# Optimization experiments

Measured on AMD Instinct MI355X. Metric: run time of the kernel, lower is better.

## Reference

```python
import jax, jax.numpy as jnp
import numpy as np

B, N, E = 64, 64, 512          # batch, objects per image, edges per image
OBJ_DIM, Q_DIM, KS = 2048, 1024, 8
HID = Q_DIM // 2               # 512


def setup_inputs() -> dict:
    key = jax.random.key(0)
    k1, k2, k3, k4, k5, k6 = jax.random.split(key, 6)
    node_feats = jax.random.normal(k1, (B, N, OBJ_DIM), jnp.float32)
    q_feats = jax.random.normal(k2, (B, Q_DIM), jnp.float32)
    # Edges: per-image random (i, j) pairs with self-loops removed, indices into
    # the flattened [B*N*N] pairwise tensor, sorted by batch (m//b per image).
    i = jax.random.randint(k3, (B, E), 0, N)
    off = jax.random.randint(k4, (B, E), 1, N)
    j = (i + off) % N
    base = jnp.arange(B)[:, None] * (N * N)
    indexes = (base + i * N + j).reshape(-1).astype(jnp.int32)  # [B*E]
    scale = 0.02
    W_obj = jax.random.normal(k5, (OBJ_DIM, HID), jnp.float32) * scale
    b_obj = jnp.zeros((HID,), jnp.float32)
    W_q = jax.random.normal(k6, (Q_DIM, HID * KS), jnp.float32) * scale
    b_q = jnp.zeros((HID * KS,), jnp.float32)
    return {"node_feats": node_feats, "q_feats": q_feats, "indexes": indexes,
            "W_obj": W_obj, "b_obj": b_obj, "W_q": W_q, "b_q": b_q}


def reference(node_feats, q_feats, indexes, W_obj, b_obj, W_q, b_q):
    b, n, _ = node_feats.shape
    # obj_prob_l: Linear + ReLU -> [B, N, HID]
    node_h = jax.nn.relu(jnp.einsum('bno,oh->bnh', node_feats, W_obj) + b_obj)
    hid = node_h.shape[-1]
    # node_intersect(method='sum') then gather via graph.indexes:
    # equivalent to gathering (i, j) pairs directly instead of materializing [B*N*N, HID]
    bidx = indexes // (n * n)
    rem = indexes % (n * n)
    src = rem // n
    dst = rem % n
    obj_e = node_h[bidx, src] + node_h[bidx, dst]            # [M, HID]
    # q_prob_l: Linear + ReLU -> [B, HID*KS], viewed as per-edge kernels [M, HID, KS]
    q_h = jax.nn.relu(q_feats @ W_q + b_q)                   # [B, HID*KS]
    ks = q_h.shape[-1] // hid
    q_e = q_h.reshape(b, hid, ks)[bidx]                      # [M, HID, KS]
    # batched (1,HID) @ (HID,KS) dot product, then divide by per-kernel norm
    edge_logit = jnp.einsum('mh,mhk->mk', obj_e, q_e)        # [M, KS]
    edge_logit = edge_logit / jnp.linalg.norm(q_e, axis=1)   # [M, KS]
    return edge_logit
```

## Files before the change

kernel.cpp:

```cpp
#include <hip/hip_runtime.h>
#include <hip/hip_bf16.h>


using bf16x8 = __attribute__((ext_vector_type(8))) __bf16;
using f32x4  = __attribute__((ext_vector_type(4))) float;

__device__ __forceinline__ unsigned short f2bf(float f) {
    unsigned int u = __float_as_uint(f);
    unsigned int r = (u + 0x7FFFu + ((u >> 16) & 1u)) >> 16;
    return (unsigned short)r;
}

__device__ __forceinline__ uint4 pk8u(f32x4 a, f32x4 b) {
    union { unsigned short us[8]; uint4 u4; } r;
    r.us[0] = f2bf(a[0]); r.us[1] = f2bf(a[1]); r.us[2] = f2bf(a[2]); r.us[3] = f2bf(a[3]);
    r.us[4] = f2bf(b[0]); r.us[5] = f2bf(b[1]); r.us[6] = f2bf(b[2]); r.us[7] = f2bf(b[3]);
    return r.u4;
}

__device__ __forceinline__ bf16x8 pk8(f32x4 a, f32x4 b) {
    union { uint4 u4; bf16x8 v; } r;
    r.u4 = pk8u(a, b);
    return r.v;
}

__device__ __forceinline__ void gl_lds16(const void* g, void* l) {
    __builtin_amdgcn_global_load_lds(
        (const __attribute__((address_space(1))) unsigned int*)g,
        (__attribute__((address_space(3))) unsigned int*)l,
        16, 0, 0);
}

__global__ __launch_bounds__(256) void cvt_k(const float* __restrict__ nf,
                                             const float* __restrict__ W,
                                             unsigned short* __restrict__ A,
                                             unsigned short* __restrict__ WT) {
    __shared__ float lds[32][33];
    int bid = blockIdx.x;
    if (bid < 2048) {
        int tid = bid * 256 + threadIdx.x;
        for (int p = tid; p < 1048576; p += 524288) {
            int r = p >> 8;
            int grp = p & 255;
            int chunk = grp >> 4, slot = grp & 15;
            int sslot = slot ^ (r & 15);
            const float* src = nf + (size_t)r * 2048 + chunk * 128 + sslot * 8;
            f32x4 v0 = *(const f32x4*)(src);
            f32x4 v1 = *(const f32x4*)(src + 4);
            *(uint4*)(A + (size_t)r * 2048 + chunk * 128 + slot * 8) = pk8u(v0, v1);
        }
    } else {
        int g = bid - 2048;
        int k0 = (g & 63) * 32, n0 = (g >> 6) * 32;
        int tx = threadIdx.x & 31, ty = threadIdx.x >> 5;
#pragma unroll
        for (int j = 0; j < 4; ++j)
            lds[ty + j * 8][tx] = W[(size_t)(k0 + ty + j * 8) * 512 + n0 + tx];
        __syncthreads();
#pragma unroll
        for (int j = 0; j < 4; ++j) {
            int n = n0 + ty + j * 8;
            int k = k0 + tx;
            int chunk = k >> 7, off = k & 127;
            int ksw = chunk * 128 + (((off >> 3) ^ (n & 15)) << 3) + (off & 7);
            WT[(size_t)n * 2048 + ksw] = f2bf(lds[tx][ty + j * 8]);
        }
    }
}

__device__ __forceinline__ void gemm1_body(char* smem, int g1, int t,
                                           const unsigned short* __restrict__ A,
                                           const unsigned short* __restrict__ BT,
                                           const float* __restrict__ bias,
                                           float* __restrict__ C) {
    unsigned short* AsmB = (unsigned short*)smem;
    unsigned short* BsmB = (unsigned short*)(smem + 32768);

    int swz = (g1 & 7) * 64 + (g1 >> 3);
    int by = swz >> 3, bx = swz & 7;
    int m0 = by * 64, n0 = bx * 64;

    int lane = t & 63, w = t >> 6;
    int wm = w >> 1, wn = w & 1;
    int l15 = lane & 15, l16 = lane >> 4;

    int srow = lane >> 4, scol = (lane & 15) * 8;
    const unsigned short* aG = A  + (size_t)(m0 + w * 16 + srow) * 2048 + scol;
    const unsigned short* bG = BT + (size_t)(n0 + w * 16 + srow) * 2048 + scol;

    f32x4 acc[2][2];
#pragma unroll
    for (int i = 0; i < 2; ++i)
#pragma unroll
        for (int j = 0; j < 2; ++j) acc[i][j] = (f32x4){0.f, 0.f, 0.f, 0.f};

#define G1_STAGE(buf, step)                                                    \
    do {                                                                       \
        int _ko = (step) * 128;                                                \
        unsigned short* _aL = AsmB + (buf) * 8192 + (w * 16) * 128;            \
        unsigned short* _bL = BsmB + (buf) * 8192 + (w * 16) * 128;            \
        _Pragma("unroll")                                                      \
        for (int _i = 0; _i < 4; ++_i) {                                       \
            gl_lds16(aG + (size_t)(_i * 4) * 2048 + _ko, _aL + (_i * 4) * 128);\
            gl_lds16(bG + (size_t)(_i * 4) * 2048 + _ko, _bL + (_i * 4) * 128);\
        }                                                                      \
    } while (0)

    G1_STAGE(0, 0);
    __syncthreads();

    for (int s = 0; s < 16; ++s) {
        int cur = s & 1;
        if (s < 15) G1_STAGE(cur ^ 1, s + 1);

        const char* Ab = (const char*)(AsmB + cur * 8192);
        const char* Bb = (const char*)(BsmB + cur * 8192);
#pragma unroll
        for (int ks = 0; ks < 4; ++ks) {
            int co = ks * 64 + l16 * 16;
            int r0 = wm * 32 + l15, r1 = r0 + 16;
            int c0n = wn * 32 + l15, c1n = c0n + 16;
            bf16x8 a0 = *(const bf16x8*)(Ab + r0 * 256 + (co ^ ((r0 & 15) << 4)));
            bf16x8 a1 = *(const bf16x8*)(Ab + r1 * 256 + (co ^ ((r1 & 15) << 4)));
            bf16x8 b0 = *(const bf16x8*)(Bb + c0n * 256 + (co ^ ((c0n & 15) << 4)));
            bf16x8 b1 = *(const bf16x8*)(Bb + c1n * 256 + (co ^ ((c1n & 15) << 4)));
            acc[0][0] = __builtin_amdgcn_mfma_f32_16x16x32_bf16(a0, b0, acc[0][0], 0, 0, 0);
            acc[0][1] = __builtin_amdgcn_mfma_f32_16x16x32_bf16(a0, b1, acc[0][1], 0, 0, 0);
            acc[1][0] = __builtin_amdgcn_mfma_f32_16x16x32_bf16(a1, b0, acc[1][0], 0, 0, 0);
            acc[1][1] = __builtin_amdgcn_mfma_f32_16x16x32_bf16(a1, b1, acc[1][1], 0, 0, 0);
        }
        __syncthreads();
    }
#undef G1_STAGE

#pragma unroll
    for (int fm = 0; fm < 2; ++fm)
#pragma unroll
        for (int fn = 0; fn < 2; ++fn) {
            int col = n0 + wn * 32 + fn * 16 + l15;
            float bv = bias[col];
#pragma unroll
            for (int j = 0; j < 4; ++j) {
                int row = m0 + wm * 32 + fm * 16 + l16 * 4 + j;
                float v = acc[fm][fn][j] + bv;
                C[(size_t)row * 512 + col] = v > 0.f ? v : 0.f;
            }
        }
}

#define LDK2 136
__device__ __forceinline__ void gemm2_body(char* smem, int bid2, int t,
                                           const float* __restrict__ qf,
                                           const float* __restrict__ Wq,
                                           float* __restrict__ part) {
    auto Asm = reinterpret_cast<unsigned short(*)[LDK2]>(smem);
    auto Bsm = reinterpret_cast<unsigned short(*)[LDK2]>(smem + 64 * LDK2 * 2);

    int lane = t & 63, w = t >> 6;
    int l15 = lane & 15, l16 = lane >> 4;
    int c0 = (bid2 & 31) * 128;
    int k0 = (bid2 >> 5) * 128;

#pragma unroll
    for (int j = 0; j < 4; ++j) {
        int g = t + j * 256;
        int row = g >> 4, kc = g & 15;
        const float* src = qf + (size_t)row * 1024 + k0 + kc * 8;
        f32x4 v0 = *(const f32x4*)(src);
        f32x4 v1 = *(const f32x4*)(src + 4);
        *(uint4*)(&Asm[row][kc * 8]) = pk8u(v0, v1);
    }
#pragma unroll
    for (int j = 0; j < 2; ++j) {
        int g = t + j * 256;
        int kg = g >> 5, cg = g & 31;
        f32x4 wv[8];
#pragma unroll
        for (int kk = 0; kk < 8; ++kk)
            wv[kk] = *(const f32x4*)(Wq + (size_t)(k0 + kg * 8 + kk) * 4096 + c0 + cg * 4);
#pragma unroll
        for (int cc = 0; cc < 4; ++cc) {
            union { unsigned short us[8]; uint4 u4; } p;
#pragma unroll
            for (int kk = 0; kk < 8; ++kk) p.us[kk] = f2bf(wv[kk][cc]);
            *(uint4*)(&Bsm[cg * 4 + cc][kg * 8]) = p.u4;
        }
    }
    __syncthreads();

    f32x4 acc[4][2];
#pragma unroll
    for (int i = 0; i < 4; ++i)
#pragma unroll
        for (int j = 0; j < 2; ++j) acc[i][j] = (f32x4){0.f, 0.f, 0.f, 0.f};

#pragma unroll
    for (int ks = 0; ks < 4; ++ks) {
        bf16x8 bfr[2];
#pragma unroll
        for (int jn = 0; jn < 2; ++jn)
            bfr[jn] = *(const bf16x8*)(&Bsm[w * 32 + jn * 16 + l15][ks * 32 + l16 * 8]);
#pragma unroll
        for (int i = 0; i < 4; ++i) {
            bf16x8 afr = *(const bf16x8*)(&Asm[i * 16 + l15][ks * 32 + l16 * 8]);
            acc[i][0] = __builtin_amdgcn_mfma_f32_16x16x32_bf16(afr, bfr[0], acc[i][0], 0, 0, 0);
            acc[i][1] = __builtin_amdgcn_mfma_f32_16x16x32_bf16(afr, bfr[1], acc[i][1], 0, 0, 0);
        }
    }

    float* pz = part + (size_t)(bid2 >> 5) * 262144;
#pragma unroll
    for (int i = 0; i < 4; ++i)
#pragma unroll
        for (int jn = 0; jn < 2; ++jn) {
            int col = c0 + w * 32 + jn * 16 + l15;
#pragma unroll
            for (int j = 0; j < 4; ++j) {
                int row = i * 16 + l16 * 4 + j;
                pz[(size_t)row * 4096 + col] = acc[i][jn][j];
            }
        }
}

__global__ __launch_bounds__(256) void gemm_fused(const unsigned short* A,
                                                  const unsigned short* BT,
                                                  const float* bias, float* C,
                                                  const float* qf, const float* Wq,
                                                  float* part) {
    __shared__ __align__(16) char smem[65536];
    int bid = blockIdx.x, t = threadIdx.x;
    if (bid < 256) gemm2_body(smem, bid, t, qf, Wq, part);
    else           gemm1_body(smem, bid - 256, t, A, BT, bias, C);
}
__global__ __launch_bounds__(256) void gemm1_only(const unsigned short* A,
                                                  const unsigned short* BT,
                                                  const float* bias, float* C) {
    __shared__ __align__(16) char smem[65536];
    gemm1_body(smem, blockIdx.x, threadIdx.x, A, BT, bias, C);
}
__global__ __launch_bounds__(256) void gemm2_only(const float* qf, const float* Wq,
                                                  float* part) {
    __shared__ __align__(16) char smem[65536];
    gemm2_body(smem, blockIdx.x, threadIdx.x, qf, Wq, part);
}

__global__ __launch_bounds__(256) void tail_k(const float* __restrict__ part,
                                              const float* __restrict__ bq,
                                              const float* __restrict__ node_h,
                                              const int* __restrict__ idxs,
                                              float* __restrict__ out) {
    __shared__ float qs[4096];
    __shared__ float red[4][8];
    __shared__ float inv[8];
    __shared__ float Pl[64][8];

    int b = blockIdx.x, t = threadIdx.x;
    int lane = t & 63, w = t >> 6;
    int l15 = lane & 15, l16 = lane >> 4;

#pragma unroll
    for (int j = 0; j < 4; ++j) {
        int c = j * 1024 + t * 4;
        f32x4 a = (f32x4){0.f, 0.f, 0.f, 0.f};
#pragma unroll
        for (int z = 0; z < 8; ++z)
            a += *(const f32x4*)(part + (size_t)z * 262144 + (size_t)b * 4096 + c);
        f32x4 bb = *(const f32x4*)(bq + c);
#pragma unroll
        for (int i = 0; i < 4; ++i) {
            float v = a[i] + bb[i];
            a[i] = v > 0.f ? v : 0.f;
        }
        *(f32x4*)(&qs[c]) = a;
    }
    __syncthreads();

    {
        const float* row = qs + t * 16;
        float sq[8] = {0.f, 0.f, 0.f, 0.f, 0.f, 0.f, 0.f, 0.f};
#pragma unroll
        for (int j = 0; j < 4; ++j) {
            f32x4 v = *(const f32x4*)(row + j * 4);
            sq[(j * 4 + 0) & 7] += v[0] * v[0];
            sq[(j * 4 + 1) & 7] += v[1] * v[1];
            sq[(j * 4 + 2) & 7] += v[2] * v[2];
            sq[(j * 4 + 3) & 7] += v[3] * v[3];
        }
#pragma unroll
        for (int k = 0; k < 8; ++k) {
            float v = sq[k];
            v += __shfl_xor(v, 1);  v += __shfl_xor(v, 2);  v += __shfl_xor(v, 4);
            v += __shfl_xor(v, 8);  v += __shfl_xor(v, 16); v += __shfl_xor(v, 32);
            sq[k] = v;
        }
        if (lane == 0) {
#pragma unroll
            for (int k = 0; k < 8; ++k) red[w][k] = sq[k];
        }
    }
    __syncthreads();
    if (t < 8) {
        float s = red[0][t] + red[1][t] + red[2][t] + red[3][t];
        inv[t] = 1.0f / sqrtf(s);
    }
    __syncthreads();

    {
        bool active = l15 < 8;
        float invv = active ? inv[l15] : 0.f;
        const float* arow = node_h + (size_t)(b * 64 + w * 16 + l15) * 512 + l16 * 8;
        f32x4 acc = (f32x4){0.f, 0.f, 0.f, 0.f};
#pragma unroll
        for (int kt = 0; kt < 16; ++kt) {
            f32x4 v0 = *(const f32x4*)(arow + kt * 32);
            f32x4 v1 = *(const f32x4*)(arow + kt * 32 + 4);
            bf16x8 af = pk8(v0, v1);
            union { unsigned short us[8]; bf16x8 v; } bqf;
#pragma unroll
            for (int i = 0; i < 8; ++i)
                bqf.us[i] = active ? f2bf(qs[kt * 256 + (l16 * 8 + i) * 8 + l15]) : 0;
            acc = __builtin_amdgcn_mfma_f32_16x16x32_bf16(af, bqf.v, acc, 0, 0, 0);
        }
        if (active) {
#pragma unroll
            for (int j = 0; j < 4; ++j)
                Pl[w * 16 + l16 * 4 + j][l15] = acc[j] * invv;
        }
    }
    __syncthreads();

#pragma unroll
    for (int e = 0; e < 2; ++e) {
        int m = b * 512 + e * 256 + t;
        int idx = idxs[m];
        int r = idx & 4095;
        int src = r >> 6, dst = r & 63;
        f32x4 o0 = *(const f32x4*)(&Pl[src][0]) + *(const f32x4*)(&Pl[dst][0]);
        f32x4 o1 = *(const f32x4*)(&Pl[src][4]) + *(const f32x4*)(&Pl[dst][4]);
        *(f32x4*)(out + (size_t)m * 8)     = o0;
        *(f32x4*)(out + (size_t)m * 8 + 4) = o1;
    }
}

extern "C" void kernel_launch(void* const* d_in, const int* in_sizes, int n_in,
                              void* d_out, int out_size, void* d_ws, size_t ws_size,
                              hipStream_t stream) {
    const float* node_feats = (const float*)d_in[0];
    const float* q_feats    = (const float*)d_in[1];
    const int*   indexes    = (const int*)d_in[2];
    const float* W_obj      = (const float*)d_in[3];
    const float* b_obj      = (const float*)d_in[4];
    const float* W_q        = (const float*)d_in[5];
    const float* b_q        = (const float*)d_in[6];
    float* out = (float*)d_out;

    char* ws = (char*)d_ws;
    unsigned short* A_swz = (unsigned short*)(ws + 0);
    unsigned short* W_T   = (unsigned short*)(ws + 16777216);
    float* node_h         = (float*)(ws + 18874368);

    if (ws_size >= 35651584ull) {
        float* part = (float*)(ws + 27262976);
        cvt_k<<<3072, 256, 0, stream>>>(node_feats, W_obj, A_swz, W_T);
        gemm_fused<<<768, 256, 0, stream>>>(A_swz, W_T, b_obj, node_h,
                                            q_feats, W_q, part);
        tail_k<<<64, 256, 0, stream>>>(part, b_q, node_h, indexes, out);
    } else {
        float* part = (float*)(ws + 0);
        cvt_k<<<3072, 256, 0, stream>>>(node_feats, W_obj, A_swz, W_T);
        gemm1_only<<<512, 256, 0, stream>>>(A_swz, W_T, b_obj, node_h);
        gemm2_only<<<256, 256, 0, stream>>>(q_feats, W_q, part);
        tail_k<<<64, 256, 0, stream>>>(part, b_q, node_h, indexes, out);
    }
}
```

Baseline: 43.18 us.

## Move q-projection GEMM into conversion kernel, run gemm1 standalone

```diff
diff --git a/kernel.cpp b/kernel.cpp
--- a/kernel.cpp
+++ b/kernel.cpp
@@ -31,14 +31,96 @@
         16, 0, 0);
 }
 
-__global__ __launch_bounds__(256) void cvt_k(const float* __restrict__ nf,
+#define LDK2 136
+__device__ __forceinline__ void gemm2_body(char* smem, int bid2, int t,
+                                           const float* __restrict__ qf,
+                                           const float* __restrict__ Wq,
+                                           float* __restrict__ part) {
+    auto Asm = reinterpret_cast<unsigned short(*)[LDK2]>(smem);
+    auto Bsm = reinterpret_cast<unsigned short(*)[LDK2]>(smem + 64 * LDK2 * 2);
+
+    int lane = t & 63, w = t >> 6;
+    int l15 = lane & 15, l16 = lane >> 4;
+    int c0 = (bid2 & 31) * 128;
+    int k0 = (bid2 >> 5) * 128;
+
+#pragma unroll
+    for (int j = 0; j < 4; ++j) {
+        int g = t + j * 256;
+        int row = g >> 4, kc = g & 15;
+        const float* src = qf + (size_t)row * 1024 + k0 + kc * 8;
+        f32x4 v0 = *(const f32x4*)(src);
+        f32x4 v1 = *(const f32x4*)(src + 4);
+        *(uint4*)(&Asm[row][kc * 8]) = pk8u(v0, v1);
+    }
+#pragma unroll
+    for (int j = 0; j < 2; ++j) {
+        int g = t + j * 256;
+        int kg = g >> 5, cg = g & 31;
+        f32x4 wv[8];
+#pragma unroll
+        for (int kk = 0; kk < 8; ++kk)
+            wv[kk] = *(const f32x4*)(Wq + (size_t)(k0 + kg * 8 + kk) * 4096 + c0 + cg * 4);
+#pragma unroll
+        for (int cc = 0; cc < 4; ++cc) {
+            union { unsigned short us[8]; uint4 u4; } p;
+#pragma unroll
+            for (int kk = 0; kk < 8; ++kk) p.us[kk] = f2bf(wv[kk][cc]);
+            *(uint4*)(&Bsm[cg * 4 + cc][kg * 8]) = p.u4;
+        }
+    }
+    __syncthreads();
+
+    f32x4 acc[4][2];
+#pragma unroll
+    for (int i = 0; i < 4; ++i)
+#pragma unroll
+        for (int j = 0; j < 2; ++j) acc[i][j] = (f32x4){0.f, 0.f, 0.f, 0.f};
+
+#pragma unroll
+    for (int ks = 0; ks < 4; ++ks) {
+        bf16x8 bfr[2];
+#pragma unroll
+        for (int jn = 0; jn < 2; ++jn)
+            bfr[jn] = *(const bf16x8*)(&Bsm[w * 32 + jn * 16 + l15][ks * 32 + l16 * 8]);
+#pragma unroll
+        for (int i = 0; i < 4; ++i) {
+            bf16x8 afr = *(const bf16x8*)(&Asm[i * 16 + l15][ks * 32 + l16 * 8]);
+            acc[i][0] = __builtin_amdgcn_mfma_f32_16x16x32_bf16(afr, bfr[0], acc[i][0], 0, 0, 0);
+            acc[i][1] = __builtin_amdgcn_mfma_f32_16x16x32_bf16(afr, bfr[1], acc[i][1], 0, 0, 0);
+        }
+    }
+
+    float* pz = part + (size_t)(bid2 >> 5) * 262144;
+#pragma unroll
+    for (int i = 0; i < 4; ++i)
+#pragma unroll
+        for (int jn = 0; jn < 2; ++jn) {
+            int col = c0 + w * 32 + jn * 16 + l15;
+#pragma unroll
+            for (int j = 0; j < 4; ++j) {
+                int row = i * 16 + l16 * 4 + j;
+                pz[(size_t)row * 4096 + col] = acc[i][jn][j];
+            }
+        }
+}
+
+__global__ __launch_bounds__(256) void pre_k(const float* __restrict__ nf,
                                              const float* __restrict__ W,
                                              unsigned short* __restrict__ A,
-                                             unsigned short* __restrict__ WT) {
-    __shared__ float lds[32][33];
-    int bid = blockIdx.x;
-    if (bid < 2048) {
-        int tid = bid * 256 + threadIdx.x;
+                                             unsigned short* __restrict__ WT,
+                                             const float* __restrict__ qf,
+                                             const float* __restrict__ Wq,
+                                             float* __restrict__ part, int g2n) {
+    __shared__ __align__(16) char smem[52224];
+    int bid = blockIdx.x, t = threadIdx.x;
+    if (bid < g2n) {
+        gemm2_body(smem, bid, t, qf, Wq, part);
+        return;
+    }
+    int cb = bid - g2n;
+    if (cb < 2048) {
+        int tid = cb * 256 + t;
         for (int p = tid; p < 1048576; p += 524288) {
             int r = p >> 8;
             int grp = p & 255;
@@ -50,9 +132,10 @@
             *(uint4*)(A + (size_t)r * 2048 + chunk * 128 + slot * 8) = pk8u(v0, v1);
         }
     } else {
-        int g = bid - 2048;
+        auto lds = reinterpret_cast<float(*)[33]>(smem);
+        int g = cb - 2048;
         int k0 = (g & 63) * 32, n0 = (g >> 6) * 32;
-        int tx = threadIdx.x & 31, ty = threadIdx.x >> 5;
+        int tx = t & 31, ty = t >> 5;
 #pragma unroll
         for (int j = 0; j < 4; ++j)
             lds[ty + j * 8][tx] = W[(size_t)(k0 + ty + j * 8) * 512 + n0 + tx];
@@ -68,18 +151,19 @@
     }
 }
 
-__device__ __forceinline__ void gemm1_body(char* smem, int g1, int t,
-                                           const unsigned short* __restrict__ A,
-                                           const unsigned short* __restrict__ BT,
-                                           const float* __restrict__ bias,
-                                           float* __restrict__ C) {
-    unsigned short* AsmB = (unsigned short*)smem;
-    unsigned short* BsmB = (unsigned short*)(smem + 32768);
-
+__global__ __launch_bounds__(256) void gemm1(const unsigned short* __restrict__ A,
+                                             const unsigned short* __restrict__ BT,
+                                             const float* __restrict__ bias,
+                                             float* __restrict__ C) {
+    __shared__ __align__(16) unsigned short AsmB[2 * 64 * 128];
+    __shared__ __align__(16) unsigned short BsmB[2 * 64 * 128];
+
+    int g1 = blockIdx.x;
     int swz = (g1 & 7) * 64 + (g1 >> 3);
     int by = swz >> 3, bx = swz & 7;
     int m0 = by * 64, n0 = bx * 64;
 
+    int t = threadIdx.x;
     int lane = t & 63, w = t >> 6;
     int wm = w >> 1, wn = w & 1;
     int l15 = lane & 15, l16 = lane >> 4;
@@ -148,99 +232,9 @@
         }
 }
 
-#define LDK2 136
-__device__ __forceinline__ void gemm2_body(char* smem, int bid2, int t,
-                                           const float* __restrict__ qf,
-                                           const float* __restrict__ Wq,
-                                           float* __restrict__ part) {
-    auto Asm = reinterpret_cast<unsigned short(*)[LDK2]>(smem);
-    auto Bsm = reinterpret_cast<unsigned short(*)[LDK2]>(smem + 64 * LDK2 * 2);
-
-    int lane = t & 63, w = t >> 6;
-    int l15 = lane & 15, l16 = lane >> 4;
-    int c0 = (bid2 & 31) * 128;
-    int k0 = (bid2 >> 5) * 128;
-
-#pragma unroll
-    for (int j = 0; j < 4; ++j) {
-        int g = t + j * 256;
-        int row = g >> 4, kc = g & 15;
-        const float* src = qf + (size_t)row * 1024 + k0 + kc * 8;
-        f32x4 v0 = *(const f32x4*)(src);
-        f32x4 v1 = *(const f32x4*)(src + 4);
-        *(uint4*)(&Asm[row][kc * 8]) = pk8u(v0, v1);
-    }
-#pragma unroll
-    for (int j = 0; j < 2; ++j) {
-        int g = t + j * 256;
-        int kg = g >> 5, cg = g & 31;
-        f32x4 wv[8];
-#pragma unroll
-        for (int kk = 0; kk < 8; ++kk)
-            wv[kk] = *(const f32x4*)(Wq + (size_t)(k0 + kg * 8 + kk) * 4096 + c0 + cg * 4);
-#pragma unroll
-        for (int cc = 0; cc < 4; ++cc) {
-            union { unsigned short us[8]; uint4 u4; } p;
-#pragma unroll
-            for (int kk = 0; kk < 8; ++kk) p.us[kk] = f2bf(wv[kk][cc]);
-            *(uint4*)(&Bsm[cg * 4 + cc][kg * 8]) = p.u4;
-        }
-    }
-    __syncthreads();
-
-    f32x4 acc[4][2];
-#pragma unroll
-    for (int i = 0; i < 4; ++i)
-#pragma unroll
-        for (int j = 0; j < 2; ++j) acc[i][j] = (f32x4){0.f, 0.f, 0.f, 0.f};
-
-#pragma unroll
-    for (int ks = 0; ks < 4; ++ks) {
-        bf16x8 bfr[2];
-#pragma unroll
-        for (int jn = 0; jn < 2; ++jn)
-            bfr[jn] = *(const bf16x8*)(&Bsm[w * 32 + jn * 16 + l15][ks * 32 + l16 * 8]);
-#pragma unroll
-        for (int i = 0; i < 4; ++i) {
-            bf16x8 afr = *(const bf16x8*)(&Asm[i * 16 + l15][ks * 32 + l16 * 8]);
-            acc[i][0] = __builtin_amdgcn_mfma_f32_16x16x32_bf16(afr, bfr[0], acc[i][0], 0, 0, 0);
-            acc[i][1] = __builtin_amdgcn_mfma_f32_16x16x32_bf16(afr, bfr[1], acc[i][1], 0, 0, 0);
-        }
-    }
-
-    float* pz = part + (size_t)(bid2 >> 5) * 262144;
-#pragma unroll
-    for (int i = 0; i < 4; ++i)
-#pragma unroll
-        for (int jn = 0; jn < 2; ++jn) {
-            int col = c0 + w * 32 + jn * 16 + l15;
-#pragma unroll
-            for (int j = 0; j < 4; ++j) {
-                int row = i * 16 + l16 * 4 + j;
-                pz[(size_t)row * 4096 + col] = acc[i][jn][j];
-            }
-        }
-}
-
-__global__ __launch_bounds__(256) void gemm_fused(const unsigned short* A,
-                                                  const unsigned short* BT,
-                                                  const float* bias, float* C,
-                                                  const float* qf, const float* Wq,
-                                                  float* part) {
-    __shared__ __align__(16) char smem[65536];
-    int bid = blockIdx.x, t = threadIdx.x;
-    if (bid < 256) gemm2_body(smem, bid, t, qf, Wq, part);
-    else           gemm1_body(smem, bid - 256, t, A, BT, bias, C);
-}
-__global__ __launch_bounds__(256) void gemm1_only(const unsigned short* A,
-                                                  const unsigned short* BT,
-                                                  const float* bias, float* C) {
-    __shared__ __align__(16) char smem[65536];
-    gemm1_body(smem, blockIdx.x, threadIdx.x, A, BT, bias, C);
-}
 __global__ __launch_bounds__(256) void gemm2_only(const float* qf, const float* Wq,
                                                   float* part) {
-    __shared__ __align__(16) char smem[65536];
+    __shared__ __align__(16) char smem[52224];
     gemm2_body(smem, blockIdx.x, threadIdx.x, qf, Wq, part);
 }
 
@@ -361,14 +355,15 @@
 
     if (ws_size >= 35651584ull) {
         float* part = (float*)(ws + 27262976);
-        cvt_k<<<3072, 256, 0, stream>>>(node_feats, W_obj, A_swz, W_T);
-        gemm_fused<<<768, 256, 0, stream>>>(A_swz, W_T, b_obj, node_h,
-                                            q_feats, W_q, part);
+        pre_k<<<3328, 256, 0, stream>>>(node_feats, W_obj, A_swz, W_T,
+                                        q_feats, W_q, part, 256);
+        gemm1<<<512, 256, 0, stream>>>(A_swz, W_T, b_obj, node_h);
         tail_k<<<64, 256, 0, stream>>>(part, b_q, node_h, indexes, out);
     } else {
         float* part = (float*)(ws + 0);
-        cvt_k<<<3072, 256, 0, stream>>>(node_feats, W_obj, A_swz, W_T);
-        gemm1_only<<<512, 256, 0, stream>>>(A_swz, W_T, b_obj, node_h);
+        pre_k<<<3072, 256, 0, stream>>>(node_feats, W_obj, A_swz, W_T,
+                                        q_feats, W_q, nullptr, 0);
+        gemm1<<<512, 256, 0, stream>>>(A_swz, W_T, b_obj, node_h);
         gemm2_only<<<256, 256, 0, stream>>>(q_feats, W_q, part);
         tail_k<<<64, 256, 0, stream>>>(part, b_q, node_h, indexes, out);
     }
```

New measurement: 49.08 us. +13.7%, slower.
